# Kernel optimization log

Hardware: AMD Instinct MI355X
Metric: run time of the kernel (lower is better)

## Reference

```python
import jax, jax.numpy as jnp
import numpy as np

# ---- static layer configuration (from init_kwargs) ----
B, CIN, COUT, WDIM = 8, 512, 512, 512
IN_SIZE, OUT_SIZE = 64, 64
CONV_K = 3
UP, DOWN = 2, 2                     # rint(tmp_fs/in_fs), rint(tmp_fs/out_fs); tmp_fs = 64*2 = 128
UP_TAPS, DOWN_TAPS = 12, 12         # filter_size * factor
TMP_FS = 128.0
IN_CUTOFF, IN_WIDTH = 32.0, 32.0    # width = 2*half_width
OUT_CUTOFF, OUT_WIDTH = 32.0, 32.0
CONV_CLAMP = 256.0
SLOPE = 0.2
ACT_GAIN = float(np.sqrt(2.0))
MAGNITUDE_EMA = 1.0                 # buffer init; input_gain = rsqrt(ema) = 1


def _kaiser_beta(numtaps, width, fs):
    a = 2.285 * (numtaps - 1) * np.pi * (width / (0.5 * fs)) + 7.95
    if a > 50:
        return 0.1102 * (a - 8.7)
    if a > 21:
        return 0.5842 * (a - 21) ** 0.4 + 0.07886 * (a - 21)
    return 0.0


def design_lowpass_filter(numtaps, cutoff, width, fs):
    # numpy re-implementation of scipy.signal.firwin(numtaps, cutoff, width=width, fs=fs)
    beta = _kaiser_beta(numtaps, width, fs)
    m = np.arange(numtaps) - (numtaps - 1) / 2.0
    c = cutoff / (fs / 2.0)
    h = c * np.sinc(c * m) * np.kaiser(numtaps, beta)
    h = h / h.sum()
    return jnp.asarray(h, jnp.float32)


def _fir_padding():
    pad_total = (OUT_SIZE - 1) * DOWN + 1
    pad_total -= (IN_SIZE + CONV_K - 1) * UP
    pad_total += UP_TAPS + DOWN_TAPS - 2
    pad_lo = (pad_total + UP) // 2
    pad_hi = pad_total - pad_lo
    return int(pad_lo), int(pad_hi)   # (9, 8)


def _dw_conv(x, k2d):
    # depthwise valid correlation with a (kh,kw) kernel shared across channels
    C = x.shape[1]
    kern = jnp.broadcast_to(k2d, (C, 1) + k2d.shape)
    return jax.lax.conv_general_dilated(
        x, kern, (1, 1), 'VALID',
        dimension_numbers=('NCHW', 'OIHW', 'NCHW'), feature_group_count=C)


def upfirdn_up(x, f, up, pad, gain):
    # zero-insert upsample, pad, separable true convolution with 1D filter f
    Bn, C, H, W = x.shape
    x = jnp.zeros((Bn, C, H, up, W, up), x.dtype).at[:, :, :, 0, :, 0].set(x)
    x = x.reshape(Bn, C, H * up, W * up)
    px0, px1, py0, py1 = pad
    x = jnp.pad(x, ((0, 0), (0, 0), (py0, py1), (px0, px1)))
    x = x * jnp.asarray(gain, x.dtype)
    fr = f[::-1]  # flip: true convolution (symmetric filter anyway)
    x = _dw_conv(x, fr[:, None])
    x = _dw_conv(x, fr[None, :])
    return x


def upfirdn_down(x, f, down):
    fr = f[::-1]
    x = _dw_conv(x, fr[:, None])
    x = _dw_conv(x, fr[None, :])
    return x[:, :, ::down, ::down]


def modulated_conv2d(x, wgt, s, input_gain):
    b = x.shape[0]
    O, I, kh, kw = wgt.shape
    # demodulate pre-normalization
    wgt = wgt * jax.lax.rsqrt(jnp.mean(jnp.square(wgt), axis=(1, 2, 3), keepdims=True))
    s = s * jax.lax.rsqrt(jnp.mean(jnp.square(s)))
    # per-sample modulation
    wb = wgt[None] * s[:, None, :, None, None]              # [B,O,I,kh,kw]
    d = jax.lax.rsqrt(jnp.sum(jnp.square(wb), axis=(2, 3, 4)) + 1e-8)
    wb = wb * d[:, :, None, None, None]
    wb = wb * jnp.asarray(input_gain, wb.dtype)
    # grouped conv: one filter bank per sample
    xg = x.reshape(1, b * I, x.shape[2], x.shape[3])
    wg = wb.reshape(b * O, I, kh, kw)
    y = jax.lax.conv_general_dilated(
        xg, wg, (1, 1), [(CONV_K - 1, CONV_K - 1)] * 2,
        dimension_numbers=('NCHW', 'OIHW', 'NCHW'), feature_group_count=b)
    return y.reshape(b, O, y.shape[2], y.shape[3])


def setup_inputs() -> dict:
    key = jax.random.key(0)
    k1, k2, k3, k4 = jax.random.split(key, 4)
    return {
        'x': jax.random.normal(k1, (B, CIN, IN_SIZE, IN_SIZE), jnp.float32),
        'w': jax.random.normal(k2, (B, WDIM), jnp.float32),
        'affine_weight': jax.random.normal(k3, (CIN, WDIM), jnp.float32),
        'affine_bias': jnp.ones((CIN,), jnp.float32),       # bias_init=1
        'conv_weight': jax.random.normal(k4, (COUT, CIN, CONV_K, CONV_K), jnp.float32),
        'conv_bias': jnp.zeros((COUT,), jnp.float32),
    }


def reference(x, w, affine_weight, affine_bias, conv_weight, conv_bias):
    # affine: FullyConnectedLayer with weight_gain = 1/sqrt(w_dim)
    styles = w @ (affine_weight.T * (1.0 / np.sqrt(WDIM))) + affine_bias
    input_gain = 1.0 / np.sqrt(MAGNITUDE_EMA)
    y = modulated_conv2d(x, conv_weight, styles, input_gain)
    # filtered_lrelu reference path
    y = y + conv_bias[None, :, None, None]
    fu = design_lowpass_filter(UP_TAPS, IN_CUTOFF, IN_WIDTH, TMP_FS)
    fd = design_lowpass_filter(DOWN_TAPS, OUT_CUTOFF, OUT_WIDTH, TMP_FS)
    plo, phi = _fir_padding()
    y = upfirdn_up(y, fu, UP, (plo, phi, plo, phi), gain=float(UP * UP))
    y = jnp.where(y >= 0, y, y * SLOPE) * ACT_GAIN
    y = jnp.clip(y, -CONV_CLAMP, CONV_CLAMP)
    y = upfirdn_down(y, fd, DOWN)   # [B, COUT, 64, 64]
    return y
```

## Files before the change

### kernel.cpp

```cpp
#include <hip/hip_runtime.h>
#include <cmath>
#include <cstdint>
#include <cstddef>

typedef _Float16 f16;
typedef _Float16 f16x2 __attribute__((ext_vector_type(2)));
typedef _Float16 f16x8 __attribute__((ext_vector_type(8)));
typedef float f32x4 __attribute__((ext_vector_type(4)));

#define BATCH 8
#define CIN   512
#define COUT  512
#define S0    64
#define S1    66
#define PADH  68
#define P_TOT (S1*S1)
#define MID   138
#define OUTS  64

struct FirParams { float fu[12]; float fd[12]; };

__device__ __forceinline__ void async16(const char* g, char* l) {
  __builtin_amdgcn_global_load_lds((const __attribute__((address_space(1))) void*)g,
                                   (__attribute__((address_space(3))) void*)l, 16, 0, 0);
}

__global__ __launch_bounds__(256) void k_styles(const float* __restrict__ w,
                                                const float* __restrict__ aw,
                                                const float* __restrict__ ab,
                                                float* __restrict__ styles,
                                                float* __restrict__ sumsq) {
  __shared__ float part[4];
  int wave = threadIdx.x >> 6, lane = threadIdx.x & 63;
  int gid = blockIdx.x*4 + wave;
  int b = gid >> 9, i = gid & 511;
  const float* wr = w + b*512;
  const float* ar = aw + (size_t)i*512;
  float acc = 0.f;
  #pragma unroll
  for (int k = 0; k < 8; ++k) acc += wr[lane + 64*k]*ar[lane + 64*k];
  for (int off = 32; off; off >>= 1) acc += __shfl_down(acc, off);
  if (lane == 0) {
    float v = acc*0.044194173824159216f + ab[i];
    styles[gid] = v;
    part[wave] = v*v;
  }
  __syncthreads();
  if (threadIdx.x == 0) atomicAdd(sumsq, part[0]+part[1]+part[2]+part[3]);
}

__global__ __launch_bounds__(256) void k_wg(const float* __restrict__ cw,
                                            f16* __restrict__ Wp,
                                            float* __restrict__ g) {
  int O = blockIdx.x;
  const float* base = cw + (size_t)O*4608;
  for (int I = threadIdx.x; I < 512; I += 256) {
    float v[9]; float s = 0.f;
    #pragma unroll
    for (int t = 0; t < 9; ++t) { v[t] = base[I*9 + t]; s += v[t]*v[t]; }
    g[(size_t)O*512 + I] = s;
    #pragma unroll
    for (int t = 0; t < 9; ++t) Wp[((size_t)O*9 + t)*512 + I] = (f16)v[t];
  }
}

__global__ __launch_bounds__(64) void k_scale(const float* __restrict__ g,
                                              const float* __restrict__ styles,
                                              const float* __restrict__ sumsq,
                                              float* __restrict__ sco) {
  int blk = blockIdx.x;
  int b = blk >> 9, O = blk & 511;
  int lane = threadIdx.x;
  const float* gr = g + (size_t)O*512;
  const float* sr = styles + b*512;
  float a1 = 0.f, a2 = 0.f;
  for (int I = lane; I < 512; I += 64) {
    float gg = gr[I], ss = sr[I];
    a1 += gg*ss*ss; a2 += gg;
  }
  for (int off = 32; off; off >>= 1) {
    a1 += __shfl_down(a1, off);
    a2 += __shfl_down(a2, off);
  }
  if (lane == 0) {
    float kf = 4096.0f / (*sumsq);
    a1 *= kf;
    float wn2 = 4608.f / a2;
    sco[blk] = sqrtf(wn2) / sqrtf(wn2*a1 + 1e-8f);
  }
}

__global__ __launch_bounds__(256) void k_xmod(const float* __restrict__ x,
                                              const float* __restrict__ styles,
                                              const float* __restrict__ sumsq,
                                              f16* __restrict__ Xm) {
  __shared__ float tile[128][65];
  int blk = blockIdx.x;
  int ic = blk & 3, ih = (blk >> 2) & 63, b = blk >> 8;
  int I0 = ic*128;
  float sc = sqrtf(4096.0f / (*sumsq));
  const float* xp = x + (((size_t)b*512 + I0)*64 + ih)*64;
  for (int idx = threadIdx.x; idx < 128*64; idx += 256) {
    int Il = idx >> 6, iw = idx & 63;
    tile[Il][iw] = xp[(size_t)Il*4096 + iw] * (styles[b*512 + I0 + Il]*sc);
  }
  __syncthreads();
  f16* op = Xm + (((size_t)b*PADH + ih + 2)*PADH + 2)*512 + I0;
  for (int idx = threadIdx.x; idx < 64*128; idx += 256) {
    int iw = idx >> 7, Il = idx & 127;
    op[(size_t)iw*512 + Il] = (f16)tile[Il][iw];
  }
}

__global__ __launch_bounds__(256) void k_halo(f16* __restrict__ Xm) {
  int pix = blockIdx.x*4 + (threadIdx.x >> 6);
  int lane = threadIdx.x & 63;
  int img = pix / 528, t = pix - img*528;
  int row, col;
  if (t < 272) { int rid = t/68; col = t - rid*68; row = (rid < 2) ? rid : 64 + rid; }
  else { int t2 = t - 272; int rid = t2 >> 2, cid = t2 & 3; row = rid + 2; col = (cid < 2) ? cid : 64 + cid; }
  float4* p = (float4*)(Xm + ((size_t)(img*PADH + row)*PADH + col)*512);
  p[lane] = make_float4(0.f, 0.f, 0.f, 0.f);
}

__global__ __launch_bounds__(256) void k_conv(const f16* __restrict__ Wp,
                                              const f16* __restrict__ Xm,
                                              const float* __restrict__ sco,
                                              const float* __restrict__ bias,
                                              f16* __restrict__ y1) {
  __shared__ f16x8 As[1024];
  __shared__ f16x8 Bs[1024];
  const int tid = threadIdx.x, lane = tid & 63, wave = tid >> 6;
  const int gid = blockIdx.x;
  const int b = gid & 7;
  const int r = gid >> 3;
  const int Oi = r / 35;
  int pi = r - Oi*35;
  if (Oi & 1) pi = 34 - pi;
  const int Ot = Oi * 128;
  const int pt0 = (pi < 34) ? pi*128 : 4228;

  const int srow = wave*32 + (lane >> 3);
  const int cglob = (lane & 7) ^ (lane >> 3);
  const char* aP[4]; const char* bP[4];
  #pragma unroll
  for (int q = 0; q < 4; ++q) {
    aP[q] = (const char*)Wp + (size_t)(Ot + srow + q*8)*9216 + cglob*16;
    int p = pt0 + srow + q*8;
    int oh = p/66, ow = p - oh*66;
    bP[q] = (const char*)Xm + (((size_t)b*PADH + oh)*PADH + ow)*1024 + cglob*16;
  }
  char* aL = (char*)As + wave*32*128;
  char* bL = (char*)Bs + wave*32*128;

  f32x4 acc[4][4] = {};
  const int wO = (wave & 1)*64, wPq = (wave >> 1)*64;
  const int m = lane & 15, quad = lane >> 4, mx = m & 7;

  for (int tap = 0; tap < 9; ++tap) {
    const int kh = tap/3, kw = tap - kh*3;
    const uint32_t bTap = (uint32_t)(kh*PADH + kw)*1024u;
    const uint32_t aTap = (uint32_t)tap*1024u;
    for (uint32_t I0b = 0; I0b < 1024; I0b += 128) {
      __syncthreads();
      #pragma unroll
      for (int q = 0; q < 4; ++q) async16(aP[q] + aTap + I0b, aL + q*1024);
      #pragma unroll
      for (int q = 0; q < 4; ++q) async16(bP[q] + bTap + I0b, bL + q*1024);
      __syncthreads();
      #pragma unroll
      for (int ks = 0; ks < 2; ++ks) {
        f16x8 af[4], bf[4];
        #pragma unroll
        for (int i = 0; i < 4; ++i)
          af[i] = As[(wO + i*16 + m)*8 + ((ks*4 + quad) ^ mx)];
        #pragma unroll
        for (int j = 0; j < 4; ++j)
          bf[j] = Bs[(wPq + j*16 + m)*8 + ((ks*4 + quad) ^ mx)];
        #pragma unroll
        for (int i = 0; i < 4; ++i)
          #pragma unroll
          for (int j = 0; j < 4; ++j)
            acc[i][j] = __builtin_amdgcn_mfma_f32_16x16x32_f16(af[i], bf[j], acc[i][j], 0, 0, 0);
      }
    }
  }

  #pragma unroll
  for (int i = 0; i < 4; ++i) {
    #pragma unroll
    for (int rr = 0; rr < 4; ++rr) {
      int orow = Ot + wO + i*16 + quad*4 + rr;
      float sc = sco[b*COUT + orow];
      float bb = bias[orow];
      f16* yrow = y1 + ((size_t)(b*COUT + orow))*P_TOT;
      #pragma unroll
      for (int j = 0; j < 4; ++j) {
        int p = pt0 + wPq + j*16 + m;
        yrow[p] = (f16)(acc[i][j][rr]*sc + bb);
      }
    }
  }
}

#define YPITCH 76
#define QPITCH 142
#define HPITCH 68
__global__ __launch_bounds__(256) void k_fir(const f16* __restrict__ y1,
                                             float* __restrict__ out,
                                             FirParams fp) {
  __shared__ float Yl[74*YPITCH];
  __shared__ float VU[16*YPITCH];
  __shared__ float Qs[16*QPITCH];
  __shared__ float Hr[32*HPITCH];
  const int tid = threadIdx.x;
  const f16* Y = y1 + (size_t)blockIdx.x * P_TOT;
  float* O = out + (size_t)blockIdx.x * (OUTS*OUTS);

  for (int i = tid; i < 74*YPITCH/2; i += 256)
    *(float2*)&Yl[2*i] = make_float2(0.f, 0.f);
  __syncthreads();
  const f16x2* Y2 = (const f16x2*)Y;
  for (int i = tid; i < 66*33; i += 256) {
    int r = i/33, d = i - 33*r;
    f16x2 v = Y2[33*r + d];
    *(float2*)&Yl[(r+4)*YPITCH + 4 + 2*d] = make_float2((float)v.x, (float)v.y);
  }
  __syncthreads();

  for (int k = 0; k < 9; ++k) {
    const int m0 = 16*k;
    const int nr = (k < 8) ? 16 : 10;
    const int npair = nr >> 1;

    for (int it = tid; it < npair*37; it += 256) {
      int p = it/37, c2 = it - 37*p;
      int T = 8*k + p;
      float e0=0.f,e1=0.f,o0=0.f,o1=0.f;
      #pragma unroll
      for (int a = 0; a < 6; ++a) {
        float2 v = *(const float2*)&Yl[(T+5-a)*YPITCH + 2*c2];
        e0 += fp.fu[2*a]*v.x;   e1 += fp.fu[2*a]*v.y;
        o0 += fp.fu[2*a+1]*v.x; o1 += fp.fu[2*a+1]*v.y;
      }
      *(float2*)&VU[(2*p)*YPITCH   + 2*c2] = make_float2(e0, e1);
      *(float2*)&VU[(2*p+1)*YPITCH + 2*c2] = make_float2(o0, o1);
    }
    __syncthreads();

    for (int it = tid; it < nr*23; it += 256) {
      int lr = it/23, ug = it - 23*lr;
      int U0 = 3*ug;
      float rv[8];
      #pragma unroll
      for (int d = 0; d < 8; ++d) rv[d] = VU[lr*YPITCH + U0 + d];
      #pragma unroll
      for (int u = 0; u < 3; ++u) {
        float e=0.f, o=0.f;
        #pragma unroll
        for (int t = 0; t < 6; ++t) {
          float v = rv[u+5-t];
          e += fp.fu[2*t]*v; o += fp.fu[2*t+1]*v;
        }
        e = (e >= 0.f ? e : 0.2f*e)*1.4142135623730951f;
        o = (o >= 0.f ? o : 0.2f*o)*1.4142135623730951f;
        e = fminf(fmaxf(e, -256.f), 256.f);
        o = fminf(fmaxf(o, -256.f), 256.f);
        *(float2*)&Qs[lr*QPITCH + 2*(U0+u)] = make_float2(e, o);
      }
    }
    __syncthreads();

    if (tid < nr*16) {
      int lr = tid >> 4, tg = tid & 15;
      float q[18];
      #pragma unroll
      for (int d = 0; d < 18; ++d) q[d] = Qs[lr*QPITCH + 8*tg + d];
      float a0=0.f,a1=0.f,a2=0.f,a3=0.f;
      #pragma unroll
      for (int j = 0; j < 12; ++j) {
        float c = fp.fd[j];
        a0 += c*q[11-j]; a1 += c*q[13-j]; a2 += c*q[15-j]; a3 += c*q[17-j];
      }
      *(float4*)&Hr[((m0+lr)&31)*HPITCH + 4*tg] = make_float4(a0,a1,a2,a3);
    }
    __syncthreads();

    if (k >= 1) {
      #pragma unroll
      for (int h = 0; h < 2; ++h) {
        int s = tid + 256*h;
        int tr = 8*(k-1) + (s >> 6), tc = s & 63;
        float acc = 0.f;
        #pragma unroll
        for (int j = 0; j < 12; ++j)
          acc += fp.fd[j]*Hr[((2*tr + 11 - j)&31)*HPITCH + tc];
        O[tr*64 + tc] = acc;
      }
    }
    __syncthreads();
  }
}

static double bessel_i0(double x) {
  double t = 0.25*x*x, sum = 1.0, term = 1.0;
  for (int k = 1; k < 64; ++k) {
    term *= t/((double)k*(double)k);
    sum += term;
    if (term < 1e-18*sum) break;
  }
  return sum;
}

static void design_lp(int numtaps, double cutoff, double width, double fs, float* out) {
  const double PI = 3.14159265358979323846;
  double a = 2.285*(numtaps - 1)*PI*(width/(0.5*fs)) + 7.95;
  double beta;
  if (a > 50.0)      beta = 0.1102*(a - 8.7);
  else if (a > 21.0) beta = 0.5842*pow(a - 21.0, 0.4) + 0.07886*(a - 21.0);
  else               beta = 0.0;
  double c = cutoff/(fs*0.5);
  double alpha = (numtaps - 1)*0.5;
  double i0b = bessel_i0(beta);
  double h[16], s = 0.0;
  for (int n = 0; n < numtaps; ++n) {
    double mm = n - alpha;
    double x = c*mm;
    double snc = (x == 0.0) ? 1.0 : sin(PI*x)/(PI*x);
    double r = mm/alpha;
    double kais = bessel_i0(beta*sqrt(fmax(0.0, 1.0 - r*r)))/i0b;
    h[n] = c*snc*kais; s += h[n];
  }
  for (int n = 0; n < numtaps; ++n) out[n] = (float)(h[n]/s);
}

extern "C" void kernel_launch(void* const* d_in, const int* in_sizes, int n_in,
                              void* d_out, int out_size, void* d_ws, size_t ws_size,
                              hipStream_t stream) {
  const float* x  = (const float*)d_in[0];
  const float* w  = (const float*)d_in[1];
  const float* aw = (const float*)d_in[2];
  const float* ab = (const float*)d_in[3];
  const float* cw = (const float*)d_in[4];
  const float* cb = (const float*)d_in[5];
  float* out = (float*)d_out;

  char* ws = (char*)d_ws;
  size_t off = 0;
  auto alloc = [&](size_t bytes) -> char* {
    char* p = ws + off;
    off = (off + bytes + 255) & ~(size_t)255;
    return p;
  };
  float* styles = (float*)alloc(4096*4);
  float* g      = (float*)alloc((size_t)512*512*4);
  float* sco    = (float*)alloc(4096*4);
  f16*   Wp     = (f16*)alloc((size_t)512*9*512*2);
  f16*   Xm     = (f16*)alloc((size_t)BATCH*PADH*PADH*512*2);
  f16*   y1     = (f16*)alloc((size_t)BATCH*COUT*P_TOT*2);
  float* sumsq  = (float*)alloc(4);
  (void)in_sizes; (void)n_in; (void)out_size; (void)ws_size;

  FirParams fp;
  design_lp(12, 32.0, 32.0, 128.0, fp.fu);
  design_lp(12, 32.0, 32.0, 128.0, fp.fd);
  for (int i = 0; i < 12; ++i) fp.fu[i] *= 2.0f;

  hipMemsetAsync(sumsq, 0, 4, stream);
  hipLaunchKernelGGL(k_styles, dim3(1024), dim3(256), 0, stream, w, aw, ab, styles, sumsq);
  hipLaunchKernelGGL(k_wg,     dim3(512),  dim3(256), 0, stream, cw, Wp, g);
  hipLaunchKernelGGL(k_scale,  dim3(4096), dim3(64),  0, stream, g, styles, sumsq, sco);
  hipLaunchKernelGGL(k_xmod,   dim3(2048), dim3(256), 0, stream, x, styles, sumsq, Xm);
  hipLaunchKernelGGL(k_halo,   dim3(1056), dim3(256), 0, stream, Xm);
  hipLaunchKernelGGL(k_conv,   dim3(1120), dim3(256), 0, stream, Wp, Xm, sco, cb, y1);
  hipLaunchKernelGGL(k_fir,    dim3(4096), dim3(256), 0, stream, y1, out, fp);
}
```

Before: 473.3 us.

## Double-buffer LDS tiles in modulated conv GEMM to overlap loads with MFMA

The conv kernel's K loop is flattened into 72 stages and the shared-memory A and B tiles are double-buffered, so the async global-to-LDS loads for the next stage are issued before computing on the current one. The goal is to hide global load latency behind MFMA work and to drop one barrier per iteration. It doubles LDS use per block, which may lower occupancy. Correctness relies on __syncthreads making the async LDS writes visible before they are read.

```diff
diff --git a/kernel.cpp b/kernel.cpp
--- a/kernel.cpp
+++ b/kernel.cpp
@@ -128,8 +128,8 @@
                                               const float* __restrict__ sco,
                                               const float* __restrict__ bias,
                                               f16* __restrict__ y1) {
-  __shared__ f16x8 As[1024];
-  __shared__ f16x8 Bs[1024];
+  __shared__ f16x8 As[2][1024];
+  __shared__ f16x8 Bs[2][1024];
   const int tid = threadIdx.x, lane = tid & 63, wave = tid >> 6;
   const int gid = blockIdx.x;
   const int b = gid & 7;
@@ -150,40 +150,54 @@
     int oh = p/66, ow = p - oh*66;
     bP[q] = (const char*)Xm + (((size_t)b*PADH + oh)*PADH + ow)*1024 + cglob*16;
   }
-  char* aL = (char*)As + wave*32*128;
-  char* bL = (char*)Bs + wave*32*128;
+  char* aL0 = (char*)&As[0][0] + wave*32*128;
+  char* aL1 = (char*)&As[1][0] + wave*32*128;
+  char* bL0 = (char*)&Bs[0][0] + wave*32*128;
+  char* bL1 = (char*)&Bs[1][0] + wave*32*128;
 
   f32x4 acc[4][4] = {};
   const int wO = (wave & 1)*64, wPq = (wave >> 1)*64;
   const int m = lane & 15, quad = lane >> 4, mx = m & 7;
 
-  for (int tap = 0; tap < 9; ++tap) {
-    const int kh = tap/3, kw = tap - kh*3;
-    const uint32_t bTap = (uint32_t)(kh*PADH + kw)*1024u;
-    const uint32_t aTap = (uint32_t)tap*1024u;
-    for (uint32_t I0b = 0; I0b < 1024; I0b += 128) {
-      __syncthreads();
-      #pragma unroll
-      for (int q = 0; q < 4; ++q) async16(aP[q] + aTap + I0b, aL + q*1024);
-      #pragma unroll
-      for (int q = 0; q < 4; ++q) async16(bP[q] + bTap + I0b, bL + q*1024);
-      __syncthreads();
-      #pragma unroll
-      for (int ks = 0; ks < 2; ++ks) {
-        f16x8 af[4], bf[4];
-        #pragma unroll
-        for (int i = 0; i < 4; ++i)
-          af[i] = As[(wO + i*16 + m)*8 + ((ks*4 + quad) ^ mx)];
+  auto stage = [&](int s, char* aL, char* bL) {
+    const int tap = s >> 3;
+    const int kh = (tap*11) >> 5, kw = tap - 3*kh;
+    const uint32_t ib = (uint32_t)(s & 7) << 7;
+    const uint32_t aOff = (uint32_t)tap*1024u + ib;
+    const uint32_t bOff = (uint32_t)(kh*PADH + kw)*1024u + ib;
+    #pragma unroll
+    for (int q = 0; q < 4; ++q) async16(aP[q] + aOff, aL + q*1024);
+    #pragma unroll
+    for (int q = 0; q < 4; ++q) async16(bP[q] + bOff, bL + q*1024);
+  };
+
+  auto compute = [&](const f16x8* Asb, const f16x8* Bsb) {
+    #pragma unroll
+    for (int ks = 0; ks < 2; ++ks) {
+      f16x8 af[4], bf[4];
+      #pragma unroll
+      for (int i = 0; i < 4; ++i)
+        af[i] = Asb[(wO + i*16 + m)*8 + ((ks*4 + quad) ^ mx)];
+      #pragma unroll
+      for (int j = 0; j < 4; ++j)
+        bf[j] = Bsb[(wPq + j*16 + m)*8 + ((ks*4 + quad) ^ mx)];
+      #pragma unroll
+      for (int i = 0; i < 4; ++i)
         #pragma unroll
         for (int j = 0; j < 4; ++j)
-          bf[j] = Bs[(wPq + j*16 + m)*8 + ((ks*4 + quad) ^ mx)];
-        #pragma unroll
-        for (int i = 0; i < 4; ++i)
-          #pragma unroll
-          for (int j = 0; j < 4; ++j)
-            acc[i][j] = __builtin_amdgcn_mfma_f32_16x16x32_f16(af[i], bf[j], acc[i][j], 0, 0, 0);
-      }
-    }
+          acc[i][j] = __builtin_amdgcn_mfma_f32_16x16x32_f16(af[i], bf[j], acc[i][j], 0, 0, 0);
+    }
+  };
+
+  stage(0, aL0, bL0);
+  __syncthreads();
+  for (int s = 0; s < 72; s += 2) {
+    stage(s + 1, aL1, bL1);
+    compute(As[0], Bs[0]);
+    __syncthreads();
+    if (s + 2 < 72) stage(s + 2, aL0, bL0);
+    compute(As[1], Bs[1]);
+    __syncthreads();
   }
 
   #pragma unroll
```

Measured after the change: 514.8 us. +8.8%, slower.

## Restructure FIR kernel into per-wave row strips with register-held vertical downsample

Applied to the files above, without the earlier changes.

The filtered-lrelu kernel is reorganized so each of the four waves independently processes a 16-output-row strip. Per-wave LDS scratch with wave-level fences replaces block-wide __syncthreads between the up-filter, activation and horizontal down-filter stages. The vertical downsample now runs from 42 register-held intermediate rows instead of a shared ring buffer. This removes most block barriers and LDS traffic, but recomputes halo rows for each wave (21 pairs vs 16) and raises register pressure.

```diff
diff --git a/kernel.cpp b/kernel.cpp
--- a/kernel.cpp
+++ b/kernel.cpp
@@ -23,6 +23,11 @@
 __device__ __forceinline__ void async16(const char* g, char* l) {
   __builtin_amdgcn_global_load_lds((const __attribute__((address_space(1))) void*)g,
                                    (__attribute__((address_space(3))) void*)l, 16, 0, 0);
+}
+
+__device__ __forceinline__ void wave_fence() {
+  __builtin_amdgcn_wave_barrier();
+  asm volatile("" ::: "memory");
 }
 
 __global__ __launch_bounds__(256) void k_styles(const float* __restrict__ w,
@@ -204,16 +209,16 @@
 }
 
 #define YPITCH 76
-#define QPITCH 142
-#define HPITCH 68
+#define VIX(c) ((c) + ((c) >> 4))
+#define QIX(c) ((c) + ((c) >> 4))
 __global__ __launch_bounds__(256) void k_fir(const f16* __restrict__ y1,
                                              float* __restrict__ out,
                                              FirParams fp) {
   __shared__ float Yl[74*YPITCH];
-  __shared__ float VU[16*YPITCH];
-  __shared__ float Qs[16*QPITCH];
-  __shared__ float Hr[32*HPITCH];
+  __shared__ float2 VUw[4][80];
+  __shared__ float2 Qw[4][152];
   const int tid = threadIdx.x;
+  const int wave = tid >> 6, lane = tid & 63;
   const f16* Y = y1 + (size_t)blockIdx.x * P_TOT;
   float* O = out + (size_t)blockIdx.x * (OUTS*OUTS);
 
@@ -228,77 +233,94 @@
   }
   __syncthreads();
 
-  for (int k = 0; k < 9; ++k) {
-    const int m0 = 16*k;
-    const int nr = (k < 8) ? 16 : 10;
-    const int npair = nr >> 1;
-
-    for (int it = tid; it < npair*37; it += 256) {
-      int p = it/37, c2 = it - 37*p;
-      int T = 8*k + p;
-      float e0=0.f,e1=0.f,o0=0.f,o1=0.f;
+  float2* vu = VUw[wave];
+  float2* q2 = Qw[wave];
+  float hreg[42];
+
+  #pragma unroll
+  for (int p = 0; p < 21; ++p) {
+    const int T = 16*wave + p;
+
+    {
+      float e = 0.f, o = 0.f;
       #pragma unroll
       for (int a = 0; a < 6; ++a) {
-        float2 v = *(const float2*)&Yl[(T+5-a)*YPITCH + 2*c2];
-        e0 += fp.fu[2*a]*v.x;   e1 += fp.fu[2*a]*v.y;
-        o0 += fp.fu[2*a+1]*v.x; o1 += fp.fu[2*a+1]*v.y;
-      }
-      *(float2*)&VU[(2*p)*YPITCH   + 2*c2] = make_float2(e0, e1);
-      *(float2*)&VU[(2*p+1)*YPITCH + 2*c2] = make_float2(o0, o1);
-    }
-    __syncthreads();
-
-    for (int it = tid; it < nr*23; it += 256) {
-      int lr = it/23, ug = it - 23*lr;
-      int U0 = 3*ug;
-      float rv[8];
-      #pragma unroll
-      for (int d = 0; d < 8; ++d) rv[d] = VU[lr*YPITCH + U0 + d];
-      #pragma unroll
-      for (int u = 0; u < 3; ++u) {
-        float e=0.f, o=0.f;
+        float v = Yl[(T+5-a)*YPITCH + lane];
+        e += fp.fu[2*a]*v; o += fp.fu[2*a+1]*v;
+      }
+      vu[VIX(lane)] = make_float2(e, o);
+      if (lane < 10) {
+        int c2 = 64 + lane;
+        float e2 = 0.f, o2 = 0.f;
+        #pragma unroll
+        for (int a = 0; a < 6; ++a) {
+          float v = Yl[(T+5-a)*YPITCH + c2];
+          e2 += fp.fu[2*a]*v; o2 += fp.fu[2*a+1]*v;
+        }
+        vu[VIX(c2)] = make_float2(e2, o2);
+      }
+    }
+    wave_fence();
+
+    {
+      float2 v[6];
+      #pragma unroll
+      for (int d = 0; d < 6; ++d) v[d] = vu[VIX(lane + d)];
+      float e0=0.f,o0=0.f,e1=0.f,o1=0.f;
+      #pragma unroll
+      for (int t = 0; t < 6; ++t) {
+        float2 vv = v[5-t];
+        e0 += fp.fu[2*t]*vv.x; o0 += fp.fu[2*t+1]*vv.x;
+        e1 += fp.fu[2*t]*vv.y; o1 += fp.fu[2*t+1]*vv.y;
+      }
+      e0 = fminf(fmaxf((e0 >= 0.f ? e0 : 0.2f*e0)*1.4142135623730951f, -256.f), 256.f);
+      o0 = fminf(fmaxf((o0 >= 0.f ? o0 : 0.2f*o0)*1.4142135623730951f, -256.f), 256.f);
+      e1 = fminf(fmaxf((e1 >= 0.f ? e1 : 0.2f*e1)*1.4142135623730951f, -256.f), 256.f);
+      o1 = fminf(fmaxf((o1 >= 0.f ? o1 : 0.2f*o1)*1.4142135623730951f, -256.f), 256.f);
+      q2[QIX(2*lane)]   = make_float2(e0, e1);
+      q2[QIX(2*lane+1)] = make_float2(o0, o1);
+      if (lane < 5) {
+        int u = 64 + lane;
+        float2 w[6];
+        #pragma unroll
+        for (int d = 0; d < 6; ++d) w[d] = vu[VIX(u + d)];
+        float f0=0.f,g0=0.f,f1=0.f,g1=0.f;
         #pragma unroll
         for (int t = 0; t < 6; ++t) {
-          float v = rv[u+5-t];
-          e += fp.fu[2*t]*v; o += fp.fu[2*t+1]*v;
+          float2 vv = w[5-t];
+          f0 += fp.fu[2*t]*vv.x; g0 += fp.fu[2*t+1]*vv.x;
+          f1 += fp.fu[2*t]*vv.y; g1 += fp.fu[2*t+1]*vv.y;
         }
-        e = (e >= 0.f ? e : 0.2f*e)*1.4142135623730951f;
-        o = (o >= 0.f ? o : 0.2f*o)*1.4142135623730951f;
-        e = fminf(fmaxf(e, -256.f), 256.f);
-        o = fminf(fmaxf(o, -256.f), 256.f);
-        *(float2*)&Qs[lr*QPITCH + 2*(U0+u)] = make_float2(e, o);
-      }
-    }
-    __syncthreads();
-
-    if (tid < nr*16) {
-      int lr = tid >> 4, tg = tid & 15;
-      float q[18];
-      #pragma unroll
-      for (int d = 0; d < 18; ++d) q[d] = Qs[lr*QPITCH + 8*tg + d];
-      float a0=0.f,a1=0.f,a2=0.f,a3=0.f;
+        f0 = fminf(fmaxf((f0 >= 0.f ? f0 : 0.2f*f0)*1.4142135623730951f, -256.f), 256.f);
+        g0 = fminf(fmaxf((g0 >= 0.f ? g0 : 0.2f*g0)*1.4142135623730951f, -256.f), 256.f);
+        f1 = fminf(fmaxf((f1 >= 0.f ? f1 : 0.2f*f1)*1.4142135623730951f, -256.f), 256.f);
+        g1 = fminf(fmaxf((g1 >= 0.f ? g1 : 0.2f*g1)*1.4142135623730951f, -256.f), 256.f);
+        q2[QIX(2*u)]   = make_float2(f0, f1);
+        q2[QIX(2*u+1)] = make_float2(g0, g1);
+      }
+    }
+    wave_fence();
+
+    {
+      float a0 = 0.f, a1 = 0.f;
       #pragma unroll
       for (int j = 0; j < 12; ++j) {
-        float c = fp.fd[j];
-        a0 += c*q[11-j]; a1 += c*q[13-j]; a2 += c*q[15-j]; a3 += c*q[17-j];
-      }
-      *(float4*)&Hr[((m0+lr)&31)*HPITCH + 4*tg] = make_float4(a0,a1,a2,a3);
-    }
-    __syncthreads();
-
-    if (k >= 1) {
-      #pragma unroll
-      for (int h = 0; h < 2; ++h) {
-        int s = tid + 256*h;
-        int tr = 8*(k-1) + (s >> 6), tc = s & 63;
-        float acc = 0.f;
-        #pragma unroll
-        for (int j = 0; j < 12; ++j)
-          acc += fp.fd[j]*Hr[((2*tr + 11 - j)&31)*HPITCH + tc];
-        O[tr*64 + tc] = acc;
-      }
-    }
-    __syncthreads();
+        float2 qv = q2[QIX(2*lane + 11 - j)];
+        a0 += fp.fd[j]*qv.x; a1 += fp.fd[j]*qv.y;
+      }
+      hreg[2*p]   = a0;
+      hreg[2*p+1] = a1;
+    }
+    wave_fence();
+  }
+
+  #pragma unroll
+  for (int i = 0; i < 16; ++i) {
+    float acc = 0.f;
+    #pragma unroll
+    for (int j = 0; j < 12; ++j)
+      acc += fp.fd[j]*hreg[2*i + 11 - j];
+    O[(16*wave + i)*64 + lane] = acc;
   }
 }
 
```

Measured after the change: 655.9 us. 38.6% more time.
